# Performance work log

Measured on AMD Instinct MI355X. Metric: run time of the kernel, lower is better.

## Reference

```python
import jax, jax.numpy as jnp
import numpy as np

WS = 9
PAD = WS // 2  # 4


def _unfold(x, H, W):
    # x: [N,C,H,W] -> [N,C,81,H,W], reflect-padded 9x9 windows,
    # tap order (row-major over kernel) matching torch F.unfold.
    xp = jnp.pad(x, ((0, 0), (0, 0), (PAD, PAD), (PAD, PAD)), mode='reflect')
    return jnp.stack(
        [xp[:, :, i:i + H, j:j + W] for i in range(WS) for j in range(WS)],
        axis=2,
    )


def _bilinear_align_corners(x, H, W):
    # torch F.interpolate(mode='bilinear', align_corners=True)
    N, C, h, w = x.shape
    ys = jnp.linspace(0.0, h - 1.0, H)
    xs = jnp.linspace(0.0, w - 1.0, W)
    y0 = jnp.floor(ys).astype(jnp.int32)
    x0 = jnp.floor(xs).astype(jnp.int32)
    y1 = jnp.minimum(y0 + 1, h - 1)
    x1 = jnp.minimum(x0 + 1, w - 1)
    wy = (ys - y0)[:, None]   # [H,1]
    wx = (xs - x0)[None, :]   # [1,W]
    g = lambda yi, xi: x[:, :, yi, :][:, :, :, xi]
    top = g(y0, x0) * (1.0 - wx) + g(y0, x1) * wx
    bot = g(y1, x0) * (1.0 - wx) + g(y1, x1) * wx
    return top * (1.0 - wy) + bot * wy


def setup_inputs() -> dict:
    key = jax.random.key(0)
    ks = jax.random.split(key, 6)
    N, H, W = 4, 128, 128
    return {
        'delta': jax.random.normal(ks[0], (N, 64, H, W), jnp.float32),
        'out': jax.random.normal(ks[1], (N, 2, H // 2, W // 2), jnp.float32),
        'ab_logits': jax.random.normal(ks[2], (N, 81, H * W), jnp.float32),
        'w1': jax.random.normal(ks[3], (16, 64), jnp.float32) * 0.125,
        'b1': jnp.zeros((16,), jnp.float32),
        'w2': jax.random.normal(ks[4], (16, 64), jnp.float32) * 0.125,
        'b2': jnp.zeros((16,), jnp.float32),
        'gamma_d': jnp.ones((), jnp.float32),
        'gamma_s': jnp.ones((), jnp.float32),
    }


def reference(delta, out, ab_logits, w1, b1, w2, b2, gamma_d, gamma_s):
    N, C, H, W = delta.shape
    # 1x1 convs
    f1 = jnp.einsum('nchw,oc->nohw', delta, w1) + b1[None, :, None, None]
    f2 = jnp.einsum('nchw,oc->nohw', delta, w2) + b2[None, :, None, None]
    # windowed squared-distance correlation
    f2_unf = _unfold(f2, H, W).reshape(N, 16, WS * WS, H * W)
    d_center = f1.reshape(N, 16, 1, H * W)
    delta_logits = -jnp.sum((d_center - f2_unf) ** 2, axis=1)  # [N,81,HW]
    attn = jax.nn.softmax(gamma_d * delta_logits + gamma_s * ab_logits, axis=1)
    # weighted local aggregation of (detached, upsampled) out
    out_up = _bilinear_align_corners(jax.lax.stop_gradient(out), H, W)
    out_unf = _unfold(out_up, H, W).reshape(N, 2, WS * WS, H * W)
    out_refine = jnp.sum(out_unf * attn[:, None], axis=2)  # [N,2,HW]
    return out_refine.reshape(N, 2, H, W)
```

## Files before the change

### kernel.cpp

```cpp
#include <hip/hip_runtime.h>

#define HW   16384
#define NPIX 65536

typedef _Float16 f16x2 __attribute__((ext_vector_type(2)));

#if __has_builtin(__builtin_amdgcn_fdot2)
#define DOT2(a, b, c) __builtin_amdgcn_fdot2((a), (b), (c), false)
#else
__device__ __forceinline__ float dot2_fb(f16x2 a, f16x2 b, float c) {
    return fmaf((float)a.x, (float)b.x, fmaf((float)a.y, (float)b.y, c));
}
#define DOT2(a, b, c) dot2_fb((a), (b), (c))
#endif

#if __has_builtin(__builtin_amdgcn_exp2f)
#define EXP2F(x) __builtin_amdgcn_exp2f(x)
#else
#define EXP2F(x) exp2f(x)
#endif

__device__ __forceinline__ unsigned packh2(float a, float b) {
    f16x2 h; h.x = (_Float16)a; h.y = (_Float16)b;
    return __builtin_bit_cast(unsigned, h);
}
__device__ __forceinline__ f16x2 bch(unsigned u) {
    return __builtin_bit_cast(f16x2, u);
}

__global__ __launch_bounds__(256) void pass1_kernel(
    const float* __restrict__ delta, const float* __restrict__ outlo,
    const float* __restrict__ w1, const float* __restrict__ b1,
    const float* __restrict__ w2, const float* __restrict__ b2,
    uint4* __restrict__ f1p4, uint4* __restrict__ f2p4, float2* __restrict__ recp)
{
    const int m = blockIdx.y;
    const int g = blockIdx.x * 256 + threadIdx.x;
    const int n = g >> 14;
    const int p = g & (HW - 1);

    const float* __restrict__ wm = m ? w2 : w1;
    const float* __restrict__ bm = m ? b2 : b1;

    float d[64];
    const float* db = delta + (size_t)n * 64 * HW + p;
#pragma unroll
    for (int c = 0; c < 64; ++c) d[c] = db[(size_t)c * HW];

    float acc[16];
#pragma unroll
    for (int o = 0; o < 16; ++o) {
        float a = bm[o];
        const float* wr = wm + o * 64;
#pragma unroll
        for (int c = 0; c < 64; ++c) a = fmaf(wr[c], d[c], a);
        acc[o] = a;
    }

    uint4* dst = m ? f2p4 : f1p4;
    uint4 q;
    q.x = packh2(acc[0], acc[1]);   q.y = packh2(acc[2], acc[3]);
    q.z = packh2(acc[4], acc[5]);   q.w = packh2(acc[6], acc[7]);
    dst[g] = q;
    q.x = packh2(acc[8], acc[9]);   q.y = packh2(acc[10], acc[11]);
    q.z = packh2(acc[12], acc[13]); q.w = packh2(acc[14], acc[15]);
    dst[NPIX + g] = q;

    if (m) {
        float f2sq = 0.f;
#pragma unroll
        for (int o = 0; o < 16; ++o) f2sq = fmaf(acc[o], acc[o], f2sq);

        const int y = p >> 7, x = p & 127;
        const float ys = (float)(y * 63) / 127.0f;
        const float xs = (float)(x * 63) / 127.0f;
        const int iy0 = (int)ys, ix0 = (int)xs;
        const float fy = ys - (float)iy0, fx = xs - (float)ix0;
        const int iy1 = min(iy0 + 1, 63), ix1 = min(ix0 + 1, 63);
        const float* ob = outlo + n * 2 * 4096;
        float o01[2];
#pragma unroll
        for (int cc = 0; cc < 2; ++cc) {
            const float* oc = ob + cc * 4096;
            const float v00 = oc[iy0*64+ix0], v01 = oc[iy0*64+ix1];
            const float v10 = oc[iy1*64+ix0], v11 = oc[iy1*64+ix1];
            const float top = v00 + fx * (v01 - v00);
            const float bot = v10 + fx * (v11 - v10);
            o01[cc] = top + fy * (bot - top);
        }
        float2 rc;
        rc.x = __builtin_bit_cast(float, packh2(o01[0], o01[1]));
        rc.y = f2sq;
        recp[g] = rc;
    }
}

__global__ __launch_bounds__(512) void pass2_kernel(
    const uint4* __restrict__ f1p4, const uint4* __restrict__ f2p4,
    const float2* __restrict__ recp, const float* __restrict__ ab,
    const float* __restrict__ gdp, const float* __restrict__ gsp,
    float* __restrict__ outp)
{
    __shared__ uint4  shA[12 * 72];
    __shared__ uint4  shB[12 * 72];
    __shared__ float2 shC[12 * 72];
    __shared__ float  shP[6 * 4 * 128];

    const int t = threadIdx.x;
    const int n = blockIdx.z;
    const int bx = blockIdx.x * 64, by = blockIdx.y * 4;

    const int w   = t >> 6;
    const int wh  = w & 3;
    const int pyr = w >> 2;
    const int px  = t & 63;
    const int pairid = pyr * 64 + px;
    const int p0 = (by + pyr * 2) * 128 + bx + px;
    const int g0 = n * HW + p0;

    const float* abn = ab + (size_t)n * 81 * HW;
    const int nrows = (wh < 2) ? 3 : 2;
    float a0v[3][9], a1v[3][9];
#pragma unroll
    for (int r = 0; r < 3; ++r) {
        if (r < nrows) {
            const int dyc = wh + r * 4;
            if (dyc <= 8) {
                const float* pp = abn + (size_t)(dyc * 9) * HW + p0;
#pragma unroll
                for (int j = 0; j < 9; ++j) a0v[r][j] = pp[(size_t)j * HW];
            }
            if (dyc >= 1) {
                const float* pp = abn + (size_t)((dyc - 1) * 9) * HW + p0 + 128;
#pragma unroll
                for (int j = 0; j < 9; ++j) a1v[r][j] = pp[(size_t)j * HW];
            }
        }
    }

    const uint4 A0 = f1p4[g0],       A1 = f1p4[NPIX + g0];
    const uint4 B0 = f1p4[g0 + 128], B1 = f1p4[NPIX + g0 + 128];

#pragma unroll
    for (int s = 0; s < 2; ++s) {
        const int idx = t + s * 512;
        if (idx < 864) {
            const int hy = idx / 72, hx = idx - hy * 72;
            int gy = by - 4 + hy; gy = gy < 0 ? -gy : (gy > 127 ? 254 - gy : gy);
            int gx = bx - 4 + hx; gx = gx < 0 ? -gx : (gx > 127 ? 254 - gx : gx);
            const int gg = n * HW + gy * 128 + gx;
            shA[idx] = f2p4[gg];
            shB[idx] = f2p4[NPIX + gg];
            shC[idx] = recp[gg];
        }
    }
    __syncthreads();

    const float gd = gdp[0], gs = gsp[0];
    const float L2E = 1.44269504088896f;
    const float g2 = 2.0f * gd * L2E, mg = -gd * L2E, gsl = gs * L2E;

    f16x2 f1a[8], f1b[8];
    f1a[0]=bch(A0.x); f1a[1]=bch(A0.y); f1a[2]=bch(A0.z); f1a[3]=bch(A0.w);
    f1a[4]=bch(A1.x); f1a[5]=bch(A1.y); f1a[6]=bch(A1.z); f1a[7]=bch(A1.w);
    f1b[0]=bch(B0.x); f1b[1]=bch(B0.y); f1b[2]=bch(B0.z); f1b[3]=bch(B0.w);
    f1b[4]=bch(B1.x); f1b[5]=bch(B1.y); f1b[6]=bch(B1.z); f1b[7]=bch(B1.w);
    float f1sqa = 0.f, f1sqb = 0.f;
#pragma unroll
    for (int k = 0; k < 8; ++k) {
        f1sqa = DOT2(f1a[k], f1a[k], f1sqa);
        f1sqb = DOT2(f1b[k], f1b[k], f1sqb);
    }
    const float c0a = mg * f1sqa;
    const float c0b = mg * f1sqb;

    float s0 = 0.f, x00 = 0.f, x01 = 0.f;
    float s1 = 0.f, x10 = 0.f, x11 = 0.f;

#pragma unroll
    for (int r = 0; r < 3; ++r) {
        if (r < nrows) {
            const int dyc = wh + r * 4;
            const bool has0 = (dyc <= 8);
            const bool has1 = (dyc >= 1);
            const int rib = (pyr * 2 + dyc) * 72 + px;
#pragma unroll
            for (int j = 0; j < 9; ++j) {
                const uint4  q0 = shA[rib + j];
                const uint4  q1 = shB[rib + j];
                const float2 rc = shC[rib + j];
                const f16x2 v0 = bch(q0.x), v1 = bch(q0.y), v2 = bch(q0.z), v3 = bch(q0.w);
                const f16x2 v4 = bch(q1.x), v5 = bch(q1.y), v6 = bch(q1.z), v7 = bch(q1.w);
                const f16x2 oh = bch(__builtin_bit_cast(unsigned, rc.x));
                const float o0f = (float)oh.x, o1f = (float)oh.y;
                const float f2s = rc.y;
                if (has0) {
                    float dt = DOT2(f1a[0], v0, 0.f);
                    dt = DOT2(f1a[1], v1, dt); dt = DOT2(f1a[2], v2, dt);
                    dt = DOT2(f1a[3], v3, dt); dt = DOT2(f1a[4], v4, dt);
                    dt = DOT2(f1a[5], v5, dt); dt = DOT2(f1a[6], v6, dt);
                    dt = DOT2(f1a[7], v7, dt);
                    float e = fmaf(g2, dt, c0a);
                    e = fmaf(mg, f2s, e);
                    e = fmaf(gsl, a0v[r][j], e);
                    const float wgt = EXP2F(e);
                    s0 += wgt; x00 = fmaf(wgt, o0f, x00); x01 = fmaf(wgt, o1f, x01);
                }
                if (has1) {
                    float dt = DOT2(f1b[0], v0, 0.f);
                    dt = DOT2(f1b[1], v1, dt); dt = DOT2(f1b[2], v2, dt);
                    dt = DOT2(f1b[3], v3, dt); dt = DOT2(f1b[4], v4, dt);
                    dt = DOT2(f1b[5], v5, dt); dt = DOT2(f1b[6], v6, dt);
                    dt = DOT2(f1b[7], v7, dt);
                    float e = fmaf(g2, dt, c0b);
                    e = fmaf(mg, f2s, e);
                    e = fmaf(gsl, a1v[r][j], e);
                    const float wgt = EXP2F(e);
                    s1 += wgt; x10 = fmaf(wgt, o0f, x10); x11 = fmaf(wgt, o1f, x11);
                }
            }
        }
    }

    shP[(0 * 4 + wh) * 128 + pairid] = s0;
    shP[(1 * 4 + wh) * 128 + pairid] = x00;
    shP[(2 * 4 + wh) * 128 + pairid] = x01;
    shP[(3 * 4 + wh) * 128 + pairid] = s1;
    shP[(4 * 4 + wh) * 128 + pairid] = x10;
    shP[(5 * 4 + wh) * 128 + pairid] = x11;
    __syncthreads();

    if (t < 128) {
        float v[6];
#pragma unroll
        for (int k = 0; k < 6; ++k) {
            const float* pp = &shP[k * 512 + t];
            v[k] = (pp[0] + pp[128]) + (pp[256] + pp[384]);
        }
        const int qx = t & 63, qyr = t >> 6;
        const int pp0 = (by + qyr * 2) * 128 + bx + qx;
        const float i0 = 1.0f / v[0], i1 = 1.0f / v[3];
        float* o0 = outp + (size_t)(n * 2 + 0) * HW;
        float* o1 = outp + (size_t)(n * 2 + 1) * HW;
        o0[pp0]       = v[1] * i0;
        o1[pp0]       = v[2] * i0;
        o0[pp0 + 128] = v[4] * i1;
        o1[pp0 + 128] = v[5] * i1;
    }
}

extern "C" void kernel_launch(void* const* d_in, const int* in_sizes, int n_in,
                              void* d_out, int out_size, void* d_ws, size_t ws_size,
                              hipStream_t stream) {
    const float* delta = (const float*)d_in[0];
    const float* outlo = (const float*)d_in[1];
    const float* ab    = (const float*)d_in[2];
    const float* w1    = (const float*)d_in[3];
    const float* b1    = (const float*)d_in[4];
    const float* w2    = (const float*)d_in[5];
    const float* b2    = (const float*)d_in[6];
    const float* gd    = (const float*)d_in[7];
    const float* gs    = (const float*)d_in[8];
    float* outp = (float*)d_out;

    uint4*  f1p4 = (uint4*)d_ws;
    uint4*  f2p4 = f1p4 + (size_t)2 * NPIX;
    float2* recp = (float2*)(f2p4 + (size_t)2 * NPIX);

    pass1_kernel<<<dim3(256, 2), dim3(256), 0, stream>>>(delta, outlo, w1, b1, w2, b2,
                                                         f1p4, f2p4, recp);
    pass2_kernel<<<dim3(2, 32, 4), dim3(512), 0, stream>>>(f1p4, f2p4, recp, ab,
                                                           gd, gs, outp);
}
```

Before: 114.0 us.

## Split 1x1 conv channels across threads and shrink pass2 tiles to one row pair

Pass1 now computes both convolutions in one launch. Each group of 64 threads handles a quarter of the input channels, and the partial sums are reduced through shared memory, so delta is read once instead of twice and each thread holds fewer registers. Pass2 drops from four output rows to two per block, with the 9 window rows spread over 8 waves. This doubles the number of blocks and cuts the halo and shared-memory footprint. The cost is a shared-memory reduction and barrier in pass1, plus proportionally more halo reloading in pass2.

```diff
diff --git a/kernel.cpp b/kernel.cpp
--- a/kernel.cpp
+++ b/kernel.cpp
@@ -34,64 +34,98 @@
     const float* __restrict__ w2, const float* __restrict__ b2,
     uint4* __restrict__ f1p4, uint4* __restrict__ f2p4, float2* __restrict__ recp)
 {
-    const int m = blockIdx.y;
-    const int g = blockIdx.x * 256 + threadIdx.x;
-    const int n = g >> 14;
-    const int p = g & (HW - 1);
-
-    const float* __restrict__ wm = m ? w2 : w1;
-    const float* __restrict__ bm = m ? b2 : b1;
-
-    float d[64];
+    __shared__ float4 shW[32][64];
+
+    const int t  = threadIdx.x;
+    const int px = t & 63, cc = t >> 6;
+    const int g0 = blockIdx.x * 64;
+    const int n  = g0 >> 14;
+    const int p  = (g0 & (HW - 1)) + px;
+
+    float d[16];
     const float* db = delta + (size_t)n * 64 * HW + p;
 #pragma unroll
-    for (int c = 0; c < 64; ++c) d[c] = db[(size_t)c * HW];
-
-    float acc[16];
+    for (int j = 0; j < 16; ++j) d[j] = db[(size_t)(cc * 16 + j) * HW];
+
+    float a1[16], a2[16];
+    const float* wr1 = w1 + cc * 16;
+    const float* wr2 = w2 + cc * 16;
 #pragma unroll
     for (int o = 0; o < 16; ++o) {
-        float a = bm[o];
-        const float* wr = wm + o * 64;
-#pragma unroll
-        for (int c = 0; c < 64; ++c) a = fmaf(wr[c], d[c], a);
-        acc[o] = a;
-    }
-
-    uint4* dst = m ? f2p4 : f1p4;
-    uint4 q;
-    q.x = packh2(acc[0], acc[1]);   q.y = packh2(acc[2], acc[3]);
-    q.z = packh2(acc[4], acc[5]);   q.w = packh2(acc[6], acc[7]);
-    dst[g] = q;
-    q.x = packh2(acc[8], acc[9]);   q.y = packh2(acc[10], acc[11]);
-    q.z = packh2(acc[12], acc[13]); q.w = packh2(acc[14], acc[15]);
-    dst[NPIX + g] = q;
-
-    if (m) {
-        float f2sq = 0.f;
-#pragma unroll
-        for (int o = 0; o < 16; ++o) f2sq = fmaf(acc[o], acc[o], f2sq);
-
-        const int y = p >> 7, x = p & 127;
-        const float ys = (float)(y * 63) / 127.0f;
-        const float xs = (float)(x * 63) / 127.0f;
-        const int iy0 = (int)ys, ix0 = (int)xs;
-        const float fy = ys - (float)iy0, fx = xs - (float)ix0;
-        const int iy1 = min(iy0 + 1, 63), ix1 = min(ix0 + 1, 63);
-        const float* ob = outlo + n * 2 * 4096;
-        float o01[2];
-#pragma unroll
-        for (int cc = 0; cc < 2; ++cc) {
-            const float* oc = ob + cc * 4096;
-            const float v00 = oc[iy0*64+ix0], v01 = oc[iy0*64+ix1];
-            const float v10 = oc[iy1*64+ix0], v11 = oc[iy1*64+ix1];
-            const float top = v00 + fx * (v01 - v00);
-            const float bot = v10 + fx * (v11 - v10);
-            o01[cc] = top + fy * (bot - top);
-        }
-        float2 rc;
-        rc.x = __builtin_bit_cast(float, packh2(o01[0], o01[1]));
-        rc.y = f2sq;
-        recp[g] = rc;
+        float s1 = 0.f, s2 = 0.f;
+        const float* q1 = wr1 + o * 64;
+        const float* q2 = wr2 + o * 64;
+#pragma unroll
+        for (int j = 0; j < 16; ++j) {
+            s1 = fmaf(q1[j], d[j], s1);
+            s2 = fmaf(q2[j], d[j], s2);
+        }
+        a1[o] = s1; a2[o] = s2;
+    }
+
+#pragma unroll
+    for (int o4 = 0; o4 < 4; ++o4) {
+        shW[cc * 4 + o4][px]       = make_float4(a1[o4*4], a1[o4*4+1], a1[o4*4+2], a1[o4*4+3]);
+        shW[16 + cc * 4 + o4][px]  = make_float4(a2[o4*4], a2[o4*4+1], a2[o4*4+2], a2[o4*4+3]);
+    }
+    __syncthreads();
+
+    if (t < 128) {
+        const int m = t >> 6, qx = t & 63;
+        const float* bm = m ? b2 : b1;
+        float acc[16];
+#pragma unroll
+        for (int o4 = 0; o4 < 4; ++o4) {
+            float4 s = shW[m * 16 + o4][qx];
+#pragma unroll
+            for (int c = 1; c < 4; ++c) {
+                const float4 v = shW[m * 16 + c * 4 + o4][qx];
+                s.x += v.x; s.y += v.y; s.z += v.z; s.w += v.w;
+            }
+            acc[o4*4]   = s.x + bm[o4*4];
+            acc[o4*4+1] = s.y + bm[o4*4+1];
+            acc[o4*4+2] = s.z + bm[o4*4+2];
+            acc[o4*4+3] = s.w + bm[o4*4+3];
+        }
+
+        const int g = g0 + qx;
+        uint4* dst = m ? f2p4 : f1p4;
+        uint4 q;
+        q.x = packh2(acc[0], acc[1]);   q.y = packh2(acc[2], acc[3]);
+        q.z = packh2(acc[4], acc[5]);   q.w = packh2(acc[6], acc[7]);
+        dst[g] = q;
+        q.x = packh2(acc[8], acc[9]);   q.y = packh2(acc[10], acc[11]);
+        q.z = packh2(acc[12], acc[13]); q.w = packh2(acc[14], acc[15]);
+        dst[NPIX + g] = q;
+
+        if (m) {
+            float f2sq = 0.f;
+#pragma unroll
+            for (int o = 0; o < 16; ++o) f2sq = fmaf(acc[o], acc[o], f2sq);
+
+            const int pq = g & (HW - 1);
+            const int y = pq >> 7, x = pq & 127;
+            const float ys = (float)(y * 63) / 127.0f;
+            const float xs = (float)(x * 63) / 127.0f;
+            const int iy0 = (int)ys, ix0 = (int)xs;
+            const float fy = ys - (float)iy0, fx = xs - (float)ix0;
+            const int iy1 = min(iy0 + 1, 63), ix1 = min(ix0 + 1, 63);
+            const float* ob = outlo + n * 2 * 4096;
+            float o01[2];
+#pragma unroll
+            for (int ch = 0; ch < 2; ++ch) {
+                const float* oc = ob + ch * 4096;
+                const float v00 = oc[iy0*64+ix0], v01 = oc[iy0*64+ix1];
+                const float v10 = oc[iy1*64+ix0], v11 = oc[iy1*64+ix1];
+                const float top = v00 + fx * (v01 - v00);
+                const float bot = v10 + fx * (v11 - v10);
+                o01[ch] = top + fy * (bot - top);
+            }
+            float2 rc;
+            rc.x = __builtin_bit_cast(float, packh2(o01[0], o01[1]));
+            rc.y = f2sq;
+            recp[g] = rc;
+        }
     }
 }
 
@@ -101,30 +135,27 @@
     const float* __restrict__ gdp, const float* __restrict__ gsp,
     float* __restrict__ outp)
 {
-    __shared__ uint4  shA[12 * 72];
-    __shared__ uint4  shB[12 * 72];
-    __shared__ float2 shC[12 * 72];
-    __shared__ float  shP[6 * 4 * 128];
+    __shared__ uint4  shA[10 * 72];
+    __shared__ uint4  shB[10 * 72];
+    __shared__ float2 shC[10 * 72];
+    __shared__ float  shP[6 * 8 * 64];
 
     const int t = threadIdx.x;
     const int n = blockIdx.z;
-    const int bx = blockIdx.x * 64, by = blockIdx.y * 4;
-
-    const int w   = t >> 6;
-    const int wh  = w & 3;
-    const int pyr = w >> 2;
-    const int px  = t & 63;
-    const int pairid = pyr * 64 + px;
-    const int p0 = (by + pyr * 2) * 128 + bx + px;
+    const int bx = blockIdx.x * 64, y0 = blockIdx.y * 2;
+
+    const int wh = t >> 6;
+    const int px = t & 63;
+    const int p0 = y0 * 128 + bx + px;
     const int g0 = n * HW + p0;
 
     const float* abn = ab + (size_t)n * 81 * HW;
-    const int nrows = (wh < 2) ? 3 : 2;
-    float a0v[3][9], a1v[3][9];
-#pragma unroll
-    for (int r = 0; r < 3; ++r) {
-        if (r < nrows) {
-            const int dyc = wh + r * 4;
+    const int nr = (wh < 2) ? 2 : 1;
+    float a0v[2][9], a1v[2][9];
+#pragma unroll
+    for (int r = 0; r < 2; ++r) {
+        if (r < nr) {
+            const int dyc = wh + r * 8;
             if (dyc <= 8) {
                 const float* pp = abn + (size_t)(dyc * 9) * HW + p0;
 #pragma unroll
@@ -144,9 +175,9 @@
 #pragma unroll
     for (int s = 0; s < 2; ++s) {
         const int idx = t + s * 512;
-        if (idx < 864) {
+        if (idx < 720) {
             const int hy = idx / 72, hx = idx - hy * 72;
-            int gy = by - 4 + hy; gy = gy < 0 ? -gy : (gy > 127 ? 254 - gy : gy);
+            int gy = y0 - 4 + hy; gy = gy < 0 ? -gy : (gy > 127 ? 254 - gy : gy);
             int gx = bx - 4 + hx; gx = gx < 0 ? -gx : (gx > 127 ? 254 - gx : gx);
             const int gg = n * HW + gy * 128 + gx;
             shA[idx] = f2p4[gg];
@@ -178,12 +209,12 @@
     float s1 = 0.f, x10 = 0.f, x11 = 0.f;
 
 #pragma unroll
-    for (int r = 0; r < 3; ++r) {
-        if (r < nrows) {
-            const int dyc = wh + r * 4;
+    for (int r = 0; r < 2; ++r) {
+        if (r < nr) {
+            const int dyc = wh + r * 8;
             const bool has0 = (dyc <= 8);
             const bool has1 = (dyc >= 1);
-            const int rib = (pyr * 2 + dyc) * 72 + px;
+            const int rib = dyc * 72 + px;
 #pragma unroll
             for (int j = 0; j < 9; ++j) {
                 const uint4  q0 = shA[rib + j];
@@ -222,23 +253,23 @@
         }
     }
 
-    shP[(0 * 4 + wh) * 128 + pairid] = s0;
-    shP[(1 * 4 + wh) * 128 + pairid] = x00;
-    shP[(2 * 4 + wh) * 128 + pairid] = x01;
-    shP[(3 * 4 + wh) * 128 + pairid] = s1;
-    shP[(4 * 4 + wh) * 128 + pairid] = x10;
-    shP[(5 * 4 + wh) * 128 + pairid] = x11;
+    shP[(0 * 8 + wh) * 64 + px] = s0;
+    shP[(1 * 8 + wh) * 64 + px] = x00;
+    shP[(2 * 8 + wh) * 64 + px] = x01;
+    shP[(3 * 8 + wh) * 64 + px] = s1;
+    shP[(4 * 8 + wh) * 64 + px] = x10;
+    shP[(5 * 8 + wh) * 64 + px] = x11;
     __syncthreads();
 
-    if (t < 128) {
+    if (t < 64) {
         float v[6];
 #pragma unroll
         for (int k = 0; k < 6; ++k) {
             const float* pp = &shP[k * 512 + t];
-            v[k] = (pp[0] + pp[128]) + (pp[256] + pp[384]);
-        }
-        const int qx = t & 63, qyr = t >> 6;
-        const int pp0 = (by + qyr * 2) * 128 + bx + qx;
+            v[k] = ((pp[0] + pp[64]) + (pp[128] + pp[192]))
+                 + ((pp[256] + pp[320]) + (pp[384] + pp[448]));
+        }
+        const int pp0 = y0 * 128 + bx + t;
         const float i0 = 1.0f / v[0], i1 = 1.0f / v[3];
         float* o0 = outp + (size_t)(n * 2 + 0) * HW;
         float* o1 = outp + (size_t)(n * 2 + 1) * HW;
@@ -267,8 +298,8 @@
     uint4*  f2p4 = f1p4 + (size_t)2 * NPIX;
     float2* recp = (float2*)(f2p4 + (size_t)2 * NPIX);
 
-    pass1_kernel<<<dim3(256, 2), dim3(256), 0, stream>>>(delta, outlo, w1, b1, w2, b2,
-                                                         f1p4, f2p4, recp);
-    pass2_kernel<<<dim3(2, 32, 4), dim3(512), 0, stream>>>(f1p4, f2p4, recp, ab,
+    pass1_kernel<<<dim3(1024), dim3(256), 0, stream>>>(delta, outlo, w1, b1, w2, b2,
+                                                       f1p4, f2p4, recp);
+    pass2_kernel<<<dim3(2, 64, 4), dim3(512), 0, stream>>>(f1p4, f2p4, recp, ab,
                                                            gd, gs, outp);
 }
```

Measured after the change: 112.7 us. About the same (-1.1%).
